# Performance work log

Measured on AMD Instinct MI355X. Metric: run time of the kernel, lower is better.

## Reference

```python
import jax, jax.numpy as jnp
import numpy as np

B, DIM, H, W = 8, 64, 128, 128
HEADS = 8
HID = DIM * 2          # ffn_expansion_factor = 2
DCONV = DIM // 4       # partial-conv channels
EPS_LN = 1e-5
EPS_NRM = 1e-12

def _conv(x, w, groups=1):
    # stride-1 conv, SAME padding (matches padding=1 for k=3, padding=0 for k=1)
    return jax.lax.conv_general_dilated(
        x, w, (1, 1), 'SAME',
        dimension_numbers=('NCHW', 'OIHW', 'NCHW'),
        feature_group_count=groups)

def _ln_channel(x, w, b):
    # WithBias LayerNorm over channel dim (to_3d puts c last, normalize last dim)
    mu = x.mean(axis=1, keepdims=True)
    var = ((x - mu) ** 2).mean(axis=1, keepdims=True)
    return (x - mu) / jnp.sqrt(var + EPS_LN) * w[None, :, None, None] + b[None, :, None, None]

def setup_inputs() -> dict:
    key = jax.random.key(0)
    ks = jax.random.split(key, 8)
    s = 0.02
    return {
        'x': jax.random.normal(ks[0], (B, DIM, H, W), jnp.float32),
        'ln1_w': jnp.ones((DIM,), jnp.float32),
        'ln1_b': jnp.zeros((DIM,), jnp.float32),
        'qkv_w': jax.random.normal(ks[1], (3 * DIM, DIM, 1, 1), jnp.float32) * s,
        'qkv_dw_w': jax.random.normal(ks[2], (3 * DIM, 1, 3, 3), jnp.float32) * s,
        'temperature': jnp.ones((HEADS, 1, 1), jnp.float32),
        'attn_mix': jnp.ones((2,), jnp.float32),
        'proj_w': jax.random.normal(ks[3], (DIM, DIM, 1, 1), jnp.float32) * s,
        'ln2_w': jnp.ones((DIM,), jnp.float32),
        'ln2_b': jnp.zeros((DIM,), jnp.float32),
        'pconv_w': jax.random.normal(ks[4], (DCONV, DCONV, 3, 3), jnp.float32) * s,
        'pin_w': jax.random.normal(ks[5], (2 * HID, DIM, 1, 1), jnp.float32) * s,
        'dw_w': jax.random.normal(ks[6], (HID, 1, 3, 3), jnp.float32) * s,
        'pout_w': jax.random.normal(ks[7], (DIM, HID, 1, 1), jnp.float32) * s,
    }

def reference(x, ln1_w, ln1_b, qkv_w, qkv_dw_w, temperature, attn_mix,
              proj_w, ln2_w, ln2_b, pconv_w, pin_w, dw_w, pout_w):
    b, c, h, w = x.shape
    ch = c // HEADS
    # ---- TwinPeakAttention on norm1(x) ----
    y = _ln_channel(x, ln1_w, ln1_b)
    qkv = _conv(_conv(y, qkv_w), qkv_dw_w, groups=3 * c)
    q, k, v = jnp.split(qkv, 3, axis=1)
    rs = lambda t: t.reshape(b, HEADS, ch, h * w)          # b head c (h w)
    q, k, v = rs(q), rs(k), rs(v)
    q = q / jnp.maximum(jnp.linalg.norm(q, axis=-1, keepdims=True), EPS_NRM)
    k = k / jnp.maximum(jnp.linalg.norm(k, axis=-1, keepdims=True), EPS_NRM)
    scores = jnp.einsum('bhcn,bhdn->bhcd', q, k)           # [b, head, ch, ch]
    attn_sm = jax.nn.softmax(scores * temperature[None], axis=-1)
    attn_relu = jnp.maximum(scores, 0.0) ** 2
    wmix = jax.nn.softmax(attn_mix)
    attn = wmix[0] * attn_sm + wmix[1] * attn_relu
    out = jnp.einsum('bhcd,bhdn->bhcn', attn, v).reshape(b, c, h, w)
    x = x + _conv(out, proj_w)
    # ---- FDFN on norm2(x) ----
    y = _ln_channel(x, ln2_w, ln2_b)
    y = jnp.concatenate([_conv(y[:, :DCONV], pconv_w), y[:, DCONV:]], axis=1)
    y = _conv(y, pin_w)                                    # [b, 2*HID, h, w]
    a, g = jnp.split(y, 2, axis=1)
    a = _conv(a, dw_w, groups=HID)
    y = _conv(jax.nn.gelu(a, approximate=False) * g, pout_w)
    return x + y
```

## Files before the change

kernel.cpp:

```cpp
#include <hip/hip_runtime.h>
#include <math.h>

#define NPIX 16384
#define B_ 8

typedef __attribute__((ext_vector_type(4))) float f32x4;
typedef __attribute__((ext_vector_type(8))) short bf16x8;
typedef __attribute__((ext_vector_type(4))) unsigned int u32x4;

__device__ inline unsigned short f2bf(float f) {
  unsigned int u = __builtin_bit_cast(unsigned int, f);
  return (unsigned short)((u + 0x7fffu + ((u >> 16) & 1u)) >> 16);
}
__device__ inline float bf2f(unsigned short h) {
  unsigned int u = ((unsigned int)h) << 16;
  return __builtin_bit_cast(float, u);
}
__device__ inline unsigned int pack2(unsigned short a, unsigned short b) {
  return (unsigned int)a | ((unsigned int)b << 16);
}
__device__ inline f32x4 mfma16(bf16x8 a, bf16x8 b, f32x4 c) {
  return __builtin_amdgcn_mfma_f32_16x16x32_bf16(a, b, c, 0, 0, 0);
}
__device__ inline void unpack8(u32x4 u, float* f) {
#pragma unroll
  for (int i = 0; i < 4; ++i) {
    unsigned int w = u[i];
    f[2 * i]     = __builtin_bit_cast(float, w << 16);
    f[2 * i + 1] = __builtin_bit_cast(float, w & 0xffff0000u);
  }
}

__global__ __launch_bounds__(256) void k0_prep(
    const float* __restrict__ wq, const float* __restrict__ lw,
    const float* __restrict__ lb, const float* __restrict__ pin,
    const float* __restrict__ pout, unsigned short* __restrict__ wq2,
    float* __restrict__ s1, float* __restrict__ s2,
    unsigned short* __restrict__ pinb, unsigned short* __restrict__ pob) {
  int bid = blockIdx.x, t = threadIdx.x;
  if (bid == 0) {
    if (t < 192) {
      int co = t;
      float a = 0.f, bsum = 0.f;
      for (int ci = 0; ci < 64; ++ci) {
        float w = wq[co * 64 + ci];
        unsigned short hb = f2bf(w * lw[ci]);
        wq2[co * 64 + ci] = hb;
        a += bf2f(hb);
        bsum = fmaf(w, lb[ci], bsum);
      }
      s1[co] = a;
      s2[co] = bsum;
    }
  } else if (bid <= 64) {
    int i = (bid - 1) * 256 + t;
    pinb[i] = f2bf(pin[i]);
  } else {
    int i = (bid - 65) * 256 + t;
    pob[i] = f2bf(pout[i]);
  }
}

__global__ __launch_bounds__(256) void k1_qkv(
    const float* __restrict__ x, const unsigned short* __restrict__ wq2,
    const float* __restrict__ s1, const float* __restrict__ s2,
    unsigned short* __restrict__ qkv) {
  __shared__ __align__(16) unsigned char lx[64 * 128];
  __shared__ float sumL[4][64], sqL[4][64], muL[64], rsL[64];
  __shared__ __align__(16) unsigned short epi[4][16][72];
  int t = threadIdx.x, blk = blockIdx.x;
  int b = blk >> 8, hw0 = (blk & 255) * 64;
  const float* xb = x + (size_t)b * 64 * NPIX + hw0;
  int p = t & 63, g8 = t >> 6;
  float psum = 0.f, psq = 0.f;
#pragma unroll
  for (int r = 0; r < 2; ++r) {
    int ci0 = g8 * 8 + r * 32;
    float v[8];
#pragma unroll
    for (int j = 0; j < 8; ++j) {
      v[j] = xb[(size_t)(ci0 + j) * NPIX + p];
      psum += v[j];
      psq = fmaf(v[j], v[j], psq);
    }
    u32x4 pk;
#pragma unroll
    for (int j = 0; j < 4; ++j) pk[j] = pack2(f2bf(v[2 * j]), f2bf(v[2 * j + 1]));
    unsigned int addr = ((unsigned)(p * 128 + ci0 * 2)) ^ ((p & 7) << 4);
    *(u32x4*)&lx[addr] = pk;
  }
  sumL[g8][p] = psum;
  sqL[g8][p] = psq;
  __syncthreads();
  if (t < 64) {
    float s = sumL[0][t] + sumL[1][t] + sumL[2][t] + sumL[3][t];
    float q = sqL[0][t] + sqL[1][t] + sqL[2][t] + sqL[3][t];
    float mu = s * (1.f / 64.f);
    float var = q * (1.f / 64.f) - mu * mu;
    muL[t] = mu;
    rsL[t] = rsqrtf(fmaxf(var, 0.f) + 1e-5f);
  }
  __syncthreads();
  int lane = t & 63, wv = t >> 6, l16 = lane & 15, g = lane >> 4;
  int co0 = wv * 48;
  bf16x8 A[3][2];
#pragma unroll
  for (int ct = 0; ct < 3; ++ct) {
    int co = co0 + ct * 16 + l16;
#pragma unroll
    for (int kh = 0; kh < 2; ++kh)
      A[ct][kh] = *(const bf16x8*)(wq2 + (size_t)co * 64 + kh * 32 + g * 8);
  }
  f32x4 acc[3][4];
#pragma unroll
  for (int ct = 0; ct < 3; ++ct)
#pragma unroll
    for (int nt = 0; nt < 4; ++nt) acc[ct][nt] = (f32x4)0.f;
#pragma unroll
  for (int nt = 0; nt < 4; ++nt) {
    int pp = nt * 16 + l16;
#pragma unroll
    for (int kh = 0; kh < 2; ++kh) {
      unsigned int addr = ((unsigned)(pp * 128 + (kh * 32 + g * 8) * 2)) ^ ((pp & 7) << 4);
      bf16x8 Bf = *(const bf16x8*)&lx[addr];
#pragma unroll
      for (int ct = 0; ct < 3; ++ct) acc[ct][nt] = mfma16(A[ct][kh], Bf, acc[ct][nt]);
    }
  }
  unsigned short* ob = qkv + (size_t)b * 192 * NPIX + hw0;
#pragma unroll
  for (int ct = 0; ct < 3; ++ct) {
#pragma unroll
    for (int r = 0; r < 4; ++r) {
      int co = co0 + ct * 16 + g * 4 + r;
      float s1v = s1[co], s2v = s2[co];
#pragma unroll
      for (int nt = 0; nt < 4; ++nt) {
        int pl = nt * 16 + l16;
        float val = (acc[ct][nt][r] - muL[pl] * s1v) * rsL[pl] + s2v;
        epi[wv][g * 4 + r][pl] = f2bf(val);
      }
    }
#pragma unroll
    for (int i = 0; i < 2; ++i) {
      int chunk = i * 64 + lane, co_l = chunk >> 3, oct = chunk & 7;
      u32x4 v = *(const u32x4*)&epi[wv][co_l][oct * 8];
      *(u32x4*)(ob + (size_t)(co0 + ct * 16 + co_l) * NPIX + oct * 8) = v;
    }
  }
}

__global__ __launch_bounds__(256) void k2_dw3x3(
    const unsigned short* __restrict__ in, const float* __restrict__ w9,
    unsigned short* __restrict__ out) {
  int blk0 = blockIdx.x;
  int blk = (blk0 & 7) * 1536 + (blk0 >> 3);
  int gid = blk * 256 + threadIdx.x;
  int plane = gid >> 11;
  int o = gid & 2047;
  int h = o >> 4, w0 = (o & 15) * 8;
  int c = plane - (plane / 192) * 192;
  const float* wp = w9 + c * 9;
  float wgt[9];
#pragma unroll
  for (int j = 0; j < 9; ++j) wgt[j] = wp[j];
  const unsigned short* ip = in + (size_t)plane * NPIX;
  float row[3][10];
#pragma unroll
  for (int dy = 0; dy < 3; ++dy) {
#pragma unroll
    for (int i = 0; i < 10; ++i) row[dy][i] = 0.f;
    int hh = h + dy - 1;
    if ((unsigned)hh < 128u) {
      const unsigned short* rp = ip + hh * 128 + w0;
      u32x4 m = *(const u32x4*)rp;
      unpack8(m, &row[dy][1]);
      if (w0 > 0) row[dy][0] = bf2f(rp[-1]);
      if (w0 < 120) row[dy][9] = bf2f(rp[8]);
    }
  }
  u32x4 res;
#pragma unroll
  for (int i = 0; i < 8; i += 2) {
    float a0 = 0.f, a1 = 0.f;
#pragma unroll
    for (int dy = 0; dy < 3; ++dy)
#pragma unroll
      for (int dx = 0; dx < 3; ++dx) {
        a0 = fmaf(wgt[dy * 3 + dx], row[dy][i + dx], a0);
        a1 = fmaf(wgt[dy * 3 + dx], row[dy][i + 1 + dx], a1);
      }
    res[i >> 1] = pack2(f2bf(a0), f2bf(a1));
  }
  *(u32x4*)(out + (size_t)plane * NPIX + h * 128 + w0) = res;
}

__global__ __launch_bounds__(256) void k3a_mfma(
    const unsigned short* __restrict__ qkvd, float* __restrict__ parts) {
  __shared__ float red[4][640];
  int blk = blockIdx.x;
  int b = blk >> 6, chunk = blk & 63;
  int t = threadIdx.x;
  int lane = t & 63, wv = t >> 6, l16 = lane & 15, g = lane >> 4;
  const unsigned short* qp = qkvd + (size_t)b * 192 * NPIX;
  const unsigned short* kp = qp + (size_t)64 * NPIX;
  int n0 = chunk * 256 + wv * 64;
  f32x4 S[4], QQ[4], KK[4];
#pragma unroll
  for (int i = 0; i < 4; ++i) { S[i] = (f32x4)0.f; QQ[i] = (f32x4)0.f; KK[i] = (f32x4)0.f; }
#pragma unroll
  for (int ks = 0; ks < 2; ++ks) {
    int k0 = n0 + ks * 32 + g * 8;
    bf16x8 Q[4], K[4];
#pragma unroll
    for (int t4 = 0; t4 < 4; ++t4) {
      Q[t4] = *(const bf16x8*)(qp + (size_t)(t4 * 16 + l16) * NPIX + k0);
      K[t4] = *(const bf16x8*)(kp + (size_t)(t4 * 16 + l16) * NPIX + k0);
    }
#pragma unroll
    for (int t4 = 0; t4 < 4; ++t4) {
      S[t4]  = mfma16(Q[t4], K[t4], S[t4]);
      QQ[t4] = mfma16(Q[t4], Q[t4], QQ[t4]);
      KK[t4] = mfma16(K[t4], K[t4], KK[t4]);
    }
  }
  int hi = l16 >> 3;
#pragma unroll
  for (int t4 = 0; t4 < 4; ++t4) {
#pragma unroll
    for (int r = 0; r < 4; ++r) {
      int m = g * 4 + r;
      if ((m >> 3) == hi) {
        int head = 2 * t4 + hi;
        red[wv][head * 80 + 16 + (m & 7) * 8 + (l16 & 7)] = S[t4][r];
      }
      if (m == l16) {
        int c = t4 * 16 + l16;
        red[wv][(c >> 3) * 80 + (c & 7)] = QQ[t4][r];
        red[wv][(c >> 3) * 80 + 8 + (c & 7)] = KK[t4][r];
      }
    }
  }
  __syncthreads();
  float* pb = parts + (size_t)blk * 640;
  for (int i = t; i < 640; i += 256)
    pb[i] = red[0][i] + red[1][i] + red[2][i] + red[3][i];
}

__global__ __launch_bounds__(256) void k3bc(
    const float* __restrict__ parts, const float* __restrict__ temp,
    const float* __restrict__ mix, const float* __restrict__ pw,
    unsigned short* __restrict__ M) {
  int b = blockIdx.x, t = threadIdx.x;
  __shared__ float s[8][80];
  __shared__ float att[8][64];
  for (int i = t; i < 640; i += 256) {
    const float* pbase = parts + (size_t)b * 64 * 640 + i;
    float v = 0.f;
    for (int c = 0; c < 64; ++c) v += pbase[c * 640];
    s[i / 80][i % 80] = v;
  }
  __syncthreads();
  float m0 = fmaxf(mix[0], mix[1]);
  float e0 = expf(mix[0] - m0), e1 = expf(mix[1] - m0);
  float w0 = e0 / (e0 + e1), w1 = e1 / (e0 + e1);
  for (int i = t; i < 512; i += 256) {
    int head = i >> 6, e = i & 63, c = e >> 3, d = e & 7;
    float tt = temp[head];
    float rq = 1.f / fmaxf(sqrtf(s[head][c]), 1e-12f);
    float sc[8];
    float mx = -1e30f;
#pragma unroll
    for (int d2 = 0; d2 < 8; ++d2) {
      float rk = 1.f / fmaxf(sqrtf(s[head][8 + d2]), 1e-12f);
      sc[d2] = s[head][16 + c * 8 + d2] * rq * rk;
      mx = fmaxf(mx, sc[d2] * tt);
    }
    float sum = 0.f;
#pragma unroll
    for (int d2 = 0; d2 < 8; ++d2) sum += expf(sc[d2] * tt - mx);
    float sm = expf(sc[d] * tt - mx) / sum;
    float r = fmaxf(sc[d], 0.f);
    r = r * r;
    att[head][e] = w0 * sm + w1 * r;
  }
  __syncthreads();
  for (int i = t; i < 4096; i += 256) {
    int co = i >> 6, ci = i & 63, head = ci >> 3, d = ci & 7;
    float a = 0.f;
#pragma unroll
    for (int cc = 0; cc < 8; ++cc)
      a = fmaf(pw[co * 64 + head * 8 + cc], att[head][cc * 8 + d], a);
    M[(size_t)b * 4096 + i] = f2bf(a);
  }
}

__global__ __launch_bounds__(256) void k4_av(
    const unsigned short* __restrict__ qkvd, const unsigned short* __restrict__ Mb,
    const float* __restrict__ x, const float* __restrict__ lw,
    const float* __restrict__ lb, unsigned short* __restrict__ x1,
    unsigned short* __restrict__ y2) {
  __shared__ __align__(16) unsigned char lv[64 * 128];
  __shared__ float sumL[4][64], sqL[4][64], muL[64], rsL[64];
  int t = threadIdx.x, blk = blockIdx.x;
  int b = blk >> 8, hw0 = (blk & 255) * 64;
  const unsigned short* vb = qkvd + (size_t)b * 192 * NPIX + (size_t)128 * NPIX + hw0;
  int p = t & 63, g8 = t >> 6;
#pragma unroll
  for (int r = 0; r < 2; ++r) {
    int ci0 = g8 * 8 + r * 32;
    unsigned short hh[8];
#pragma unroll
    for (int j = 0; j < 8; ++j) hh[j] = vb[(size_t)(ci0 + j) * NPIX + p];
    u32x4 pk;
#pragma unroll
    for (int j = 0; j < 4; ++j) pk[j] = pack2(hh[2 * j], hh[2 * j + 1]);
    unsigned int addr = ((unsigned)(p * 128 + ci0 * 2)) ^ ((p & 7) << 4);
    *(u32x4*)&lv[addr] = pk;
  }
  __syncthreads();
  int lane = t & 63, wv = t >> 6, l16 = lane & 15, g = lane >> 4;
  bf16x8 A[2];
#pragma unroll
  for (int kh = 0; kh < 2; ++kh)
    A[kh] = *(const bf16x8*)(Mb + (size_t)b * 4096 + (size_t)(wv * 16 + l16) * 64 + kh * 32 + g * 8);
  f32x4 acc[4];
#pragma unroll
  for (int nt = 0; nt < 4; ++nt) acc[nt] = (f32x4)0.f;
#pragma unroll
  for (int nt = 0; nt < 4; ++nt) {
    int pp = nt * 16 + l16;
#pragma unroll
    for (int kh = 0; kh < 2; ++kh) {
      unsigned int addr = ((unsigned)(pp * 128 + (kh * 32 + g * 8) * 2)) ^ ((pp & 7) << 4);
      bf16x8 Bf = *(const bf16x8*)&lv[addr];
      acc[nt] = mfma16(A[kh], Bf, acc[nt]);
    }
  }
  const float* xb = x + (size_t)b * 64 * NPIX + hw0;
  unsigned short* x1b = x1 + (size_t)b * 64 * NPIX + hw0;
  float vals[4][4];
#pragma unroll
  for (int nt = 0; nt < 4; ++nt) {
    float ps = 0.f, pq = 0.f;
#pragma unroll
    for (int r = 0; r < 4; ++r) {
      int co = wv * 16 + g * 4 + r;
      size_t idx = (size_t)co * NPIX + nt * 16 + l16;
      float a = acc[nt][r] + xb[idx];
      vals[nt][r] = a;
      x1b[idx] = f2bf(a);
      ps += a;
      pq = fmaf(a, a, pq);
    }
    ps += __shfl_xor(ps, 16); ps += __shfl_xor(ps, 32);
    pq += __shfl_xor(pq, 16); pq += __shfl_xor(pq, 32);
    if (g == 0) { sumL[wv][nt * 16 + l16] = ps; sqL[wv][nt * 16 + l16] = pq; }
  }
  __syncthreads();
  if (t < 64) {
    float s = sumL[0][t] + sumL[1][t] + sumL[2][t] + sumL[3][t];
    float q = sqL[0][t] + sqL[1][t] + sqL[2][t] + sqL[3][t];
    float mu = s * (1.f / 64.f);
    float var = q * (1.f / 64.f) - mu * mu;
    muL[t] = mu;
    rsL[t] = rsqrtf(fmaxf(var, 0.f) + 1e-5f);
  }
  __syncthreads();
  unsigned short* y2b = y2 + (size_t)b * 64 * NPIX + hw0;
#pragma unroll
  for (int nt = 0; nt < 4; ++nt)
#pragma unroll
    for (int r = 0; r < 4; ++r) {
      int co = wv * 16 + g * 4 + r;
      int pl = nt * 16 + l16;
      float yv = (vals[nt][r] - muL[pl]) * rsL[pl] * lw[co] + lb[co];
      y2b[(size_t)co * NPIX + pl] = f2bf(yv);
    }
}

__global__ __launch_bounds__(256) void k5_pconv(
    const unsigned short* __restrict__ y2, const float* __restrict__ pcw,
    unsigned short* __restrict__ pc) {
  __shared__ unsigned short ly[16 * 120];
  int t = threadIdx.x, blk = blockIdx.x;
  int b = blk >> 8, tile = blk & 255;
  int ty = tile >> 4, tx = tile & 15;
  int h0 = ty * 8, w0 = tx * 8;
  const unsigned short* yb = y2 + (size_t)b * 64 * NPIX;
  for (int i = t; i < 1600; i += 256) {
    int ci = i / 100, r = i - ci * 100;
    int hy = r / 10, hx = r - hy * 10;
    int gh = h0 - 1 + hy, gw = w0 - 1 + hx;
    unsigned short v = 0;
    if ((unsigned)gh < 128u && (unsigned)gw < 128u) v = yb[(size_t)ci * NPIX + gh * 128 + gw];
    ly[ci * 120 + hy * 12 + hx] = v;
  }
  __syncthreads();
  int lp = t & 63;
  int py = lp >> 3, px = lp & 7;
  int cq = __builtin_amdgcn_readfirstlane(t >> 6);
  int co0 = cq * 4;
  float a0 = 0.f, a1 = 0.f, a2 = 0.f, a3 = 0.f;
  for (int ci = 0; ci < 16; ++ci) {
    float nb[9];
#pragma unroll
    for (int ky = 0; ky < 3; ++ky)
#pragma unroll
      for (int kx = 0; kx < 3; ++kx)
        nb[ky * 3 + kx] = bf2f(ly[ci * 120 + (py + ky) * 12 + px + kx]);
    const float* wp = pcw + (co0 * 16 + ci) * 9;
#pragma unroll
    for (int k = 0; k < 9; ++k) {
      a0 = fmaf(wp[k],       nb[k], a0);
      a1 = fmaf(wp[144 + k], nb[k], a1);
      a2 = fmaf(wp[288 + k], nb[k], a2);
      a3 = fmaf(wp[432 + k], nb[k], a3);
    }
  }
  size_t obase = (size_t)b * 16 * NPIX + (h0 + py) * 128 + w0 + px;
  pc[obase + (size_t)(co0 + 0) * NPIX] = f2bf(a0);
  pc[obase + (size_t)(co0 + 1) * NPIX] = f2bf(a1);
  pc[obase + (size_t)(co0 + 2) * NPIX] = f2bf(a2);
  pc[obase + (size_t)(co0 + 3) * NPIX] = f2bf(a3);
}

__global__ __launch_bounds__(256) void k6_pin(
    const unsigned short* __restrict__ pc, const unsigned short* __restrict__ y2,
    const unsigned short* __restrict__ pinb, unsigned short* __restrict__ ag) {
  __shared__ __align__(16) unsigned char bt[64 * 128];
  __shared__ __align__(16) unsigned short epi[4][16][72];
  int t = threadIdx.x, blk = blockIdx.x;
  int b = blk >> 8, hw0 = (blk & 255) * 64;
  int px = t & 63, cb = t >> 6;
  {
    const unsigned short* base = (cb == 0) ? (pc + (size_t)b * 16 * NPIX)
                                           : (y2 + (size_t)b * 64 * NPIX);
#pragma unroll
    for (int j = 0; j < 16; j += 2) {
      int ch = cb * 16 + j;
      unsigned short v0 = base[(size_t)ch * NPIX + hw0 + px];
      unsigned short v1 = base[(size_t)(ch + 1) * NPIX + hw0 + px];
      unsigned int addr = ((unsigned)(px * 128 + ch * 2)) ^ ((px & 7) << 4);
      *(unsigned int*)&bt[addr] = pack2(v0, v1);
    }
  }
  __syncthreads();
  int lane = t & 63, wv = t >> 6, l16 = lane & 15, g = lane >> 4;
  bf16x8 A[4][2];
#pragma unroll
  for (int ct = 0; ct < 4; ++ct) {
    int co = wv * 64 + ct * 16 + l16;
#pragma unroll
    for (int kh = 0; kh < 2; ++kh)
      A[ct][kh] = *(const bf16x8*)(pinb + (size_t)co * 64 + kh * 32 + g * 8);
  }
  f32x4 acc[4][4];
#pragma unroll
  for (int ct = 0; ct < 4; ++ct)
#pragma unroll
    for (int nt = 0; nt < 4; ++nt) acc[ct][nt] = (f32x4)0.f;
#pragma unroll
  for (int nt = 0; nt < 4; ++nt) {
    int pp = nt * 16 + l16;
#pragma unroll
    for (int kh = 0; kh < 2; ++kh) {
      unsigned int addr = ((unsigned)(pp * 128 + (kh * 32 + g * 8) * 2)) ^ ((pp & 7) << 4);
      bf16x8 Bf = *(const bf16x8*)&bt[addr];
#pragma unroll
      for (int ct = 0; ct < 4; ++ct) acc[ct][nt] = mfma16(A[ct][kh], Bf, acc[ct][nt]);
    }
  }
  unsigned short* ab = ag + (size_t)b * 256 * NPIX + hw0;
#pragma unroll
  for (int ct = 0; ct < 4; ++ct) {
#pragma unroll
    for (int nt = 0; nt < 4; ++nt)
#pragma unroll
      for (int r = 0; r < 4; ++r)
        epi[wv][g * 4 + r][nt * 16 + l16] = f2bf(acc[ct][nt][r]);
#pragma unroll
    for (int i = 0; i < 2; ++i) {
      int chunk = i * 64 + lane, co_l = chunk >> 3, oct = chunk & 7;
      u32x4 v = *(const u32x4*)&epi[wv][co_l][oct * 8];
      int co = wv * 64 + ct * 16 + co_l;
      *(u32x4*)(ab + (size_t)co * NPIX + oct * 8) = v;
    }
  }
}

__global__ __launch_bounds__(256) void k7_fdfn(
    const unsigned short* __restrict__ ag, const float* __restrict__ dww,
    const unsigned short* __restrict__ pob, const unsigned short* __restrict__ x1,
    float* __restrict__ out) {
  __shared__ __align__(16) unsigned char bt[64 * 256];
  __shared__ float dwl[1152];
  int t = threadIdx.x;
  int blk0 = blockIdx.x;
  int blk = (blk0 & 7) * 256 + (blk0 >> 3);
  int b = blk >> 8, rr = blk & 255;
  int row = rr >> 1, w0t = (rr & 1) * 64;
  const unsigned short* agb = ag + (size_t)b * 256 * NPIX;
  for (int i = t; i < 1152; i += 256) dwl[i] = dww[i];
  __syncthreads();
#pragma unroll 1
  for (int it = 0; it < 2; ++it) {
    int idx = it * 256 + t;
    int chp = idx >> 3, oct = idx & 7;
    int ch0 = chp * 2;
    int w0 = w0t + oct * 8;
    float rowa[2][3][10];
    float gt[2][8];
#pragma unroll
    for (int cc = 0; cc < 2; ++cc) {
      const unsigned short* ap = agb + (size_t)(ch0 + cc) * NPIX;
#pragma unroll
      for (int dy = 0; dy < 3; ++dy) {
#pragma unroll
        for (int i2 = 0; i2 < 10; ++i2) rowa[cc][dy][i2] = 0.f;
        int hh = row + dy - 1;
        if ((unsigned)hh < 128u) {
          const unsigned short* rp = ap + hh * 128 + w0;
          unpack8(*(const u32x4*)rp, &rowa[cc][dy][1]);
          if (w0 > 0) rowa[cc][dy][0] = bf2f(rp[-1]);
          if (w0 < 120) rowa[cc][dy][9] = bf2f(rp[8]);
        }
      }
      unpack8(*(const u32x4*)(agb + (size_t)(128 + ch0 + cc) * NPIX + row * 128 + w0), gt[cc]);
    }
    float wgt[2][9];
#pragma unroll
    for (int cc = 0; cc < 2; ++cc)
#pragma unroll
      for (int j = 0; j < 9; ++j) wgt[cc][j] = dwl[(ch0 + cc) * 9 + j];
#pragma unroll
    for (int i2 = 0; i2 < 8; ++i2) {
      unsigned short h2[2];
#pragma unroll
      for (int cc = 0; cc < 2; ++cc) {
        float a = 0.f;
#pragma unroll
        for (int dy = 0; dy < 3; ++dy)
#pragma unroll
          for (int dx = 0; dx < 3; ++dx)
            a = fmaf(wgt[cc][dy * 3 + dx], rowa[cc][dy][i2 + dx], a);
        float gl = 0.5f * a * (1.f + erff(a * 0.70710678118654752f)) * gt[cc][i2];
        h2[cc] = f2bf(gl);
      }
      int pxl = oct * 8 + i2;
      unsigned int f = (unsigned)(((pxl & 7) ^ (pxl >> 3)) << 4);
      unsigned int addr = (unsigned)(pxl * 256) + (((unsigned)(ch0 * 2)) ^ f);
      *(unsigned int*)&bt[addr] = pack2(h2[0], h2[1]);
    }
  }
  __syncthreads();
  int lane = t & 63, wv = t >> 6, l16 = lane & 15, g = lane >> 4;
  bf16x8 A[4];
#pragma unroll
  for (int kh = 0; kh < 4; ++kh)
    A[kh] = *(const bf16x8*)(pob + (size_t)(wv * 16 + l16) * 128 + kh * 32 + g * 8);
  f32x4 acc[4];
#pragma unroll
  for (int nt = 0; nt < 4; ++nt) acc[nt] = (f32x4)0.f;
#pragma unroll
  for (int nt = 0; nt < 4; ++nt) {
    int pp = nt * 16 + l16;
    unsigned int f = (unsigned)(((pp & 7) ^ (pp >> 3)) << 4);
#pragma unroll
    for (int kh = 0; kh < 4; ++kh) {
      unsigned int addr = (unsigned)(pp * 256) + (((unsigned)((kh * 32 + g * 8) * 2)) ^ f);
      bf16x8 Bf = *(const bf16x8*)&bt[addr];
      acc[nt] = mfma16(A[kh], Bf, acc[nt]);
    }
  }
  __syncthreads();
  float* ebuf = (float*)&bt[wv * 4096];
#pragma unroll
  for (int nt = 0; nt < 4; ++nt)
#pragma unroll
    for (int r = 0; r < 4; ++r)
      ebuf[(g * 4 + r) * 64 + nt * 16 + l16] = acc[nt][r];
  const unsigned short* x1b = x1 + (size_t)b * 64 * NPIX + row * 128 + w0t;
  float* ob = out + (size_t)b * 64 * NPIX + row * 128 + w0t;
#pragma unroll
  for (int i = 0; i < 4; ++i) {
    int chunk = i * 64 + lane;
    int co_l = chunk >> 4, q4 = (chunk & 15) * 4;
    f32x4 v = *(const f32x4*)&ebuf[co_l * 64 + q4];
    int co = wv * 16 + co_l;
    uint2 xv = *(const uint2*)(x1b + (size_t)co * NPIX + q4);
    f32x4 o;
    o[0] = v[0] + bf2f((unsigned short)(xv.x & 0xffffu));
    o[1] = v[1] + bf2f((unsigned short)(xv.x >> 16));
    o[2] = v[2] + bf2f((unsigned short)(xv.y & 0xffffu));
    o[3] = v[3] + bf2f((unsigned short)(xv.y >> 16));
    *(f32x4*)(ob + (size_t)co * NPIX + q4) = o;
  }
}

extern "C" void kernel_launch(void* const* d_in, const int* in_sizes, int n_in,
                              void* d_out, int out_size, void* d_ws, size_t ws_size,
                              hipStream_t stream) {
  const float* x       = (const float*)d_in[0];
  const float* ln1_w   = (const float*)d_in[1];
  const float* ln1_b   = (const float*)d_in[2];
  const float* qkv_w   = (const float*)d_in[3];
  const float* qkv_dww = (const float*)d_in[4];
  const float* temp    = (const float*)d_in[5];
  const float* mix     = (const float*)d_in[6];
  const float* proj_w  = (const float*)d_in[7];
  const float* ln2_w   = (const float*)d_in[8];
  const float* ln2_b   = (const float*)d_in[9];
  const float* pconv_w = (const float*)d_in[10];
  const float* pin_w   = (const float*)d_in[11];
  const float* dw_w    = (const float*)d_in[12];
  const float* pout_w  = (const float*)d_in[13];
  float* out = (float*)d_out;

  if (ws_size < (size_t)117515776) return;
  char* w8 = (char*)d_ws;
  unsigned short* qkv  = (unsigned short*)(w8 + 0);
  unsigned short* qkvd = (unsigned short*)(w8 + 50331648);
  unsigned short* x1   = (unsigned short*)(w8 + 100663296);
  unsigned short* wq2  = (unsigned short*)(w8 + 117440512);
  float*          s1   = (float*)(w8 + 117465088);
  float*          s2   = (float*)(w8 + 117465856);
  unsigned short* pinb = (unsigned short*)(w8 + 117466624);
  unsigned short* pob  = (unsigned short*)(w8 + 117499392);
  float*          parts= (float*)(w8 + 0);
  unsigned short* M    = (unsigned short*)(w8 + 2097152);
  unsigned short* y2   = (unsigned short*)(w8 + 4194304);
  unsigned short* pc   = (unsigned short*)(w8 + 20971520);
  unsigned short* ag   = (unsigned short*)(w8 + 33554432);

  k0_prep<<<97, 256, 0, stream>>>(qkv_w, ln1_w, ln1_b, pin_w, pout_w, wq2, s1, s2, pinb, pob);
  k1_qkv<<<2048, 256, 0, stream>>>(x, wq2, s1, s2, qkv);
  k2_dw3x3<<<12288, 256, 0, stream>>>(qkv, qkv_dww, qkvd);
  k3a_mfma<<<512, 256, 0, stream>>>(qkvd, parts);
  k3bc<<<8, 256, 0, stream>>>(parts, temp, mix, proj_w, M);
  k4_av<<<2048, 256, 0, stream>>>(qkvd, M, x, ln2_w, ln2_b, x1, y2);
  k5_pconv<<<2048, 256, 0, stream>>>(y2, pconv_w, pc);
  k6_pin<<<2048, 256, 0, stream>>>(pc, y2, pinb, ag);
  k7_fdfn<<<2048, 256, 0, stream>>>(ag, dw_w, pob, x1, out);
}
```

Measured before the change: 178.3 us.

## Store qkv and FFN intermediates in row-major [b,h,c,w] layout

Changes the bf16 intermediate buffers (qkv, depthwise qkv output, FFN a/g) from channel-planar [b,c,h,w] to a row-interleaved [b,h,c,w] layout, and updates every producer and consumer kernel's indexing to match. The goal is to keep each 64-pixel tile's channel rows contiguous so that epilogue stores and channel-strided loads touch nearby memory instead of striding by a full plane, improving DRAM page and cache locality. The depthwise kernel's thread mapping now iterates channel within a row. In exchange, vertical 3x3 neighbours in the depthwise kernels are now a full row of channels apart rather than 128 elements, which may reduce L2 reuse of adjacent rows.

```diff
diff --git a/kernel.cpp b/kernel.cpp
--- a/kernel.cpp
+++ b/kernel.cpp
@@ -30,6 +30,7 @@
     f[2 * i + 1] = __builtin_bit_cast(float, w & 0xffff0000u);
   }
 }
+
 
 __global__ __launch_bounds__(256) void k0_prep(
     const float* __restrict__ wq, const float* __restrict__ lw,
@@ -127,7 +128,8 @@
       for (int ct = 0; ct < 3; ++ct) acc[ct][nt] = mfma16(A[ct][kh], Bf, acc[ct][nt]);
     }
   }
-  unsigned short* ob = qkv + (size_t)b * 192 * NPIX + hw0;
+  int row1 = hw0 >> 7, wb1 = hw0 & 127;
+  unsigned short* ob = qkv + ((size_t)(b * 128 + row1) * 192) * 128 + wb1;
 #pragma unroll
   for (int ct = 0; ct < 3; ++ct) {
 #pragma unroll
@@ -145,7 +147,7 @@
     for (int i = 0; i < 2; ++i) {
       int chunk = i * 64 + lane, co_l = chunk >> 3, oct = chunk & 7;
       u32x4 v = *(const u32x4*)&epi[wv][co_l][oct * 8];
-      *(u32x4*)(ob + (size_t)(co0 + ct * 16 + co_l) * NPIX + oct * 8) = v;
+      *(u32x4*)(ob + (size_t)(co0 + ct * 16 + co_l) * 128 + oct * 8) = v;
     }
   }
 }
@@ -155,28 +157,29 @@
     unsigned short* __restrict__ out) {
   int blk0 = blockIdx.x;
   int blk = (blk0 & 7) * 1536 + (blk0 >> 3);
-  int gid = blk * 256 + threadIdx.x;
-  int plane = gid >> 11;
-  int o = gid & 2047;
-  int h = o >> 4, w0 = (o & 15) * 8;
-  int c = plane - (plane / 192) * 192;
-  const float* wp = w9 + c * 9;
+  int id = blk * 256 + threadIdx.x;
+  int oct = id & 15;
+  int cr = id >> 4;
+  int ch = cr % 192;
+  int br = cr / 192;
+  int row = br & 127;
+  int w0 = oct * 8;
+  const float* wp = w9 + ch * 9;
   float wgt[9];
 #pragma unroll
   for (int j = 0; j < 9; ++j) wgt[j] = wp[j];
-  const unsigned short* ip = in + (size_t)plane * NPIX;
-  float row[3][10];
+  float rowv[3][10];
 #pragma unroll
   for (int dy = 0; dy < 3; ++dy) {
 #pragma unroll
-    for (int i = 0; i < 10; ++i) row[dy][i] = 0.f;
-    int hh = h + dy - 1;
+    for (int i = 0; i < 10; ++i) rowv[dy][i] = 0.f;
+    int hh = row + dy - 1;
     if ((unsigned)hh < 128u) {
-      const unsigned short* rp = ip + hh * 128 + w0;
+      const unsigned short* rp = in + ((size_t)(br + dy - 1) * 192 + ch) * 128 + w0;
       u32x4 m = *(const u32x4*)rp;
-      unpack8(m, &row[dy][1]);
-      if (w0 > 0) row[dy][0] = bf2f(rp[-1]);
-      if (w0 < 120) row[dy][9] = bf2f(rp[8]);
+      unpack8(m, &rowv[dy][1]);
+      if (w0 > 0) rowv[dy][0] = bf2f(rp[-1]);
+      if (w0 < 120) rowv[dy][9] = bf2f(rp[8]);
     }
   }
   u32x4 res;
@@ -187,12 +190,12 @@
     for (int dy = 0; dy < 3; ++dy)
 #pragma unroll
       for (int dx = 0; dx < 3; ++dx) {
-        a0 = fmaf(wgt[dy * 3 + dx], row[dy][i + dx], a0);
-        a1 = fmaf(wgt[dy * 3 + dx], row[dy][i + 1 + dx], a1);
+        a0 = fmaf(wgt[dy * 3 + dx], rowv[dy][i + dx], a0);
+        a1 = fmaf(wgt[dy * 3 + dx], rowv[dy][i + 1 + dx], a1);
       }
     res[i >> 1] = pack2(f2bf(a0), f2bf(a1));
   }
-  *(u32x4*)(out + (size_t)plane * NPIX + h * 128 + w0) = res;
+  *(u32x4*)(out + ((size_t)br * 192 + ch) * 128 + w0) = res;
 }
 
 __global__ __launch_bounds__(256) void k3a_mfma(
@@ -202,8 +205,7 @@
   int b = blk >> 6, chunk = blk & 63;
   int t = threadIdx.x;
   int lane = t & 63, wv = t >> 6, l16 = lane & 15, g = lane >> 4;
-  const unsigned short* qp = qkvd + (size_t)b * 192 * NPIX;
-  const unsigned short* kp = qp + (size_t)64 * NPIX;
+  const unsigned short* bb = qkvd + (size_t)(b * 128) * 192 * 128;
   int n0 = chunk * 256 + wv * 64;
   f32x4 S[4], QQ[4], KK[4];
 #pragma unroll
@@ -211,11 +213,13 @@
 #pragma unroll
   for (int ks = 0; ks < 2; ++ks) {
     int k0 = n0 + ks * 32 + g * 8;
+    int r = k0 >> 7, w = k0 & 127;
+    const unsigned short* rowb = bb + ((size_t)r * 192) * 128 + w;
     bf16x8 Q[4], K[4];
 #pragma unroll
     for (int t4 = 0; t4 < 4; ++t4) {
-      Q[t4] = *(const bf16x8*)(qp + (size_t)(t4 * 16 + l16) * NPIX + k0);
-      K[t4] = *(const bf16x8*)(kp + (size_t)(t4 * 16 + l16) * NPIX + k0);
+      Q[t4] = *(const bf16x8*)(rowb + (size_t)(t4 * 16 + l16) * 128);
+      K[t4] = *(const bf16x8*)(rowb + (size_t)(64 + t4 * 16 + l16) * 128);
     }
 #pragma unroll
     for (int t4 = 0; t4 < 4; ++t4) {
@@ -304,14 +308,15 @@
   __shared__ float sumL[4][64], sqL[4][64], muL[64], rsL[64];
   int t = threadIdx.x, blk = blockIdx.x;
   int b = blk >> 8, hw0 = (blk & 255) * 64;
-  const unsigned short* vb = qkvd + (size_t)b * 192 * NPIX + (size_t)128 * NPIX + hw0;
+  int row4 = hw0 >> 7, wb4 = hw0 & 127;
+  const unsigned short* vb = qkvd + ((size_t)(b * 128 + row4) * 192 + 128) * 128 + wb4;
   int p = t & 63, g8 = t >> 6;
 #pragma unroll
   for (int r = 0; r < 2; ++r) {
     int ci0 = g8 * 8 + r * 32;
     unsigned short hh[8];
 #pragma unroll
-    for (int j = 0; j < 8; ++j) hh[j] = vb[(size_t)(ci0 + j) * NPIX + p];
+    for (int j = 0; j < 8; ++j) hh[j] = vb[(size_t)(ci0 + j) * 128 + p];
     u32x4 pk;
 #pragma unroll
     for (int j = 0; j < 4; ++j) pk[j] = pack2(hh[2 * j], hh[2 * j + 1]);
@@ -471,7 +476,8 @@
       for (int ct = 0; ct < 4; ++ct) acc[ct][nt] = mfma16(A[ct][kh], Bf, acc[ct][nt]);
     }
   }
-  unsigned short* ab = ag + (size_t)b * 256 * NPIX + hw0;
+  int row6 = hw0 >> 7, wb6 = hw0 & 127;
+  unsigned short* ab = ag + ((size_t)(b * 128 + row6) * 256) * 128 + wb6;
 #pragma unroll
   for (int ct = 0; ct < 4; ++ct) {
 #pragma unroll
@@ -484,7 +490,7 @@
       int chunk = i * 64 + lane, co_l = chunk >> 3, oct = chunk & 7;
       u32x4 v = *(const u32x4*)&epi[wv][co_l][oct * 8];
       int co = wv * 64 + ct * 16 + co_l;
-      *(u32x4*)(ab + (size_t)co * NPIX + oct * 8) = v;
+      *(u32x4*)(ab + (size_t)co * 128 + oct * 8) = v;
     }
   }
 }
@@ -500,7 +506,6 @@
   int blk = (blk0 & 7) * 256 + (blk0 >> 3);
   int b = blk >> 8, rr = blk & 255;
   int row = rr >> 1, w0t = (rr & 1) * 64;
-  const unsigned short* agb = ag + (size_t)b * 256 * NPIX;
   for (int i = t; i < 1152; i += 256) dwl[i] = dww[i];
   __syncthreads();
 #pragma unroll 1
@@ -513,20 +518,20 @@
     float gt[2][8];
 #pragma unroll
     for (int cc = 0; cc < 2; ++cc) {
-      const unsigned short* ap = agb + (size_t)(ch0 + cc) * NPIX;
+      int ch = ch0 + cc;
 #pragma unroll
       for (int dy = 0; dy < 3; ++dy) {
 #pragma unroll
         for (int i2 = 0; i2 < 10; ++i2) rowa[cc][dy][i2] = 0.f;
         int hh = row + dy - 1;
         if ((unsigned)hh < 128u) {
-          const unsigned short* rp = ap + hh * 128 + w0;
+          const unsigned short* rp = ag + ((size_t)(b * 128 + hh) * 256 + ch) * 128 + w0;
           unpack8(*(const u32x4*)rp, &rowa[cc][dy][1]);
           if (w0 > 0) rowa[cc][dy][0] = bf2f(rp[-1]);
           if (w0 < 120) rowa[cc][dy][9] = bf2f(rp[8]);
         }
       }
-      unpack8(*(const u32x4*)(agb + (size_t)(128 + ch0 + cc) * NPIX + row * 128 + w0), gt[cc]);
+      unpack8(*(const u32x4*)(ag + ((size_t)(b * 128 + row) * 256 + 128 + ch) * 128 + w0), gt[cc]);
     }
     float wgt[2][9];
 #pragma unroll
```

Result: no change. 175.2 us (median of 2 runs) (-1.8%).
